# Optimization experiments

Measured on AMD Instinct MI355X. Metric: run time of the kernel, lower is better.

## Reference

```python
import jax, jax.numpy as jnp
import numpy as np

N = 25000      # nodes
E = 250000     # edges (per graph)
D_IN = 256     # input feature dim
H = 4          # heads (both stages)
D = 64         # per-head out dim (hidden_size1 == hidden_size2)
NEG_SLOPE = 0.2  # DGL GATConv default leaky_relu slope


def gat_layer(x, W, al, ar, b, src, dst):
    # x: [N, F_in]; W: [F_in, H*D]; al, ar: [H, D]; b: [H*D]
    feat = (x @ W).reshape(N, H, D)                       # [N,H,D]
    el = jnp.einsum('nhd,hd->nh', feat, al)               # [N,H]
    er = jnp.einsum('nhd,hd->nh', feat, ar)               # [N,H]
    e = jax.nn.leaky_relu(el[src] + er[dst], NEG_SLOPE)   # [E,H]
    # edge softmax over incoming edges of each dst node
    m = jax.ops.segment_max(e, dst, num_segments=N)       # [N,H]
    a = jnp.exp(e - m[dst])                               # [E,H]
    s = jax.ops.segment_sum(a, dst, num_segments=N)       # [N,H]
    alpha = a / s[dst]                                    # [E,H]
    out = jax.ops.segment_sum(alpha[:, :, None] * feat[src], dst, num_segments=N)  # [N,H,D]
    return jax.nn.relu(out + b.reshape(1, H, D))


def dot_score(h, u, v):
    # u_dot_v over last dim: h [N,H,D] -> score [E,H,1]
    return jnp.sum(h[u] * h[v], axis=-1, keepdims=True)


def setup_inputs() -> dict:
    key = jax.random.key(0)
    ks = jax.random.split(key, 16)
    x = jax.random.normal(ks[0], (N, D_IN), dtype=jnp.float32)
    src = jax.random.randint(ks[1], (E,), 0, N, dtype=jnp.int32)
    dst = jax.random.randint(ks[2], (E,), 0, N, dtype=jnp.int32)
    neg_src = jax.random.randint(ks[3], (E,), 0, N, dtype=jnp.int32)
    neg_dst = jax.random.randint(ks[4], (E,), 0, N, dtype=jnp.int32)
    sc = 0.1
    params = {}
    fin = D_IN
    for i in range(3):
        k = 5 + 3 * i
        params[f'W{i+1}'] = sc * jax.random.normal(ks[k], (fin, H * D), dtype=jnp.float32)
        params[f'al{i+1}'] = sc * jax.random.normal(ks[k + 1], (H, D), dtype=jnp.float32)
        params[f'ar{i+1}'] = sc * jax.random.normal(ks[k + 2], (H, D), dtype=jnp.float32)
        params[f'b{i+1}'] = jnp.zeros((H * D,), dtype=jnp.float32)
        fin = H * D
    return dict(x=x, src=src, dst=dst, neg_src=neg_src, neg_dst=neg_dst, **params)


def reference(x, src, dst, neg_src, neg_dst,
              W1, al1, ar1, b1, W2, al2, ar2, b2, W3, al3, ar3, b3):
    h = gat_layer(x, W1, al1, ar1, b1, src, dst)
    h = gat_layer(h.reshape(N, -1), W2, al2, ar2, b2, src, dst)
    h = gat_layer(h.reshape(N, -1), W3, al3, ar3, b3, src, dst)  # [N,H,D]
    return dot_score(h, src, dst), dot_score(h, neg_src, neg_dst)
```

## Files before the change

### kernel.cpp

```cpp
#include <hip/hip_runtime.h>
#include <hip/hip_bf16.h>
#include <math.h>

#define N_NODES 25000
#define N_EDGES 250000
#define NH 4
#define F 256
#define NEG_SLOPE 0.2f

typedef float  f32x4 __attribute__((ext_vector_type(4)));
typedef short  s16x8 __attribute__((ext_vector_type(8)));
typedef ushort u16x8 __attribute__((ext_vector_type(8)));

__device__ inline ushort f2bf(float f) {
    uint u = __float_as_uint(f);
    u += 0x7FFF + ((u >> 16) & 1);
    return (ushort)(u >> 16);
}
__device__ inline float bf2f(ushort s) { return __uint_as_float(((uint)s) << 16); }

__global__ __launch_bounds__(256) void k_cast(const float* __restrict__ x,
                                              ushort* __restrict__ xb) {
    int i = blockIdx.x * blockDim.x + threadIdx.x;
    if (i * 4 >= N_NODES * F) return;
    float4 v = *(const float4*)&x[i * 4];
    ushort4 o;
    o.x = f2bf(v.x); o.y = f2bf(v.y); o.z = f2bf(v.z); o.w = f2bf(v.w);
    *(ushort4*)&xb[i * 4] = o;
}

__global__ void k_degree(const int* __restrict__ dst, int* deg) {
    int e = blockIdx.x * blockDim.x + threadIdx.x;
    if (e < N_EDGES) atomicAdd(&deg[dst[e]], 1);
}

__global__ __launch_bounds__(1024) void k_scan(const int* __restrict__ deg, int* rowptr) {
    __shared__ int sums[1024];
    const int CH = 25;
    int t = threadIdx.x;
    int base = t * CH;
    int s = 0;
    for (int i = 0; i < CH; ++i) {
        int idx = base + i;
        if (idx < N_NODES) s += deg[idx];
    }
    sums[t] = s;
    __syncthreads();
    for (int off = 1; off < 1024; off <<= 1) {
        int v = (t >= off) ? sums[t - off] : 0;
        __syncthreads();
        sums[t] += v;
        __syncthreads();
    }
    int prefix = (t == 0) ? 0 : sums[t - 1];
    for (int i = 0; i < CH; ++i) {
        int idx = base + i;
        if (idx < N_NODES) {
            rowptr[idx] = prefix;
            prefix += deg[idx];
        }
    }
    if (t == 1023) rowptr[N_NODES] = prefix;
}

__global__ void k_bucket(const int* __restrict__ src, const int* __restrict__ dst,
                         const int* __restrict__ rowptr, int* cursor, int* esrc) {
    int e = blockIdx.x * blockDim.x + threadIdx.x;
    if (e >= N_EDGES) return;
    int d = dst[e];
    int p = atomicAdd(&cursor[d], 1);
    esrc[rowptr[d] + p] = src[e];
}

__global__ __launch_bounds__(256) void k_wprep(const float* __restrict__ W,
        short* __restrict__ Hi, short* __restrict__ Lo) {
    __shared__ float T[64][65];
    int bk = (blockIdx.x & 3) * 64;
    int bn = (blockIdx.x >> 2) * 64;
    int t = threadIdx.x;
    int r = t >> 6, c = t & 63;
    #pragma unroll
    for (int i = 0; i < 64; i += 4)
        T[r + i][c] = W[(bk + r + i) * 256 + bn + c];
    __syncthreads();
    #pragma unroll
    for (int i = 0; i < 64; i += 4) {
        float w = T[c][r + i];
        ushort h = f2bf(w);
        Hi[(bn + r + i) * 256 + bk + c] = (short)h;
        Lo[(bn + r + i) * 256 + bk + c] = (short)f2bf(w - bf2f(h));
    }
}

__global__ __launch_bounds__(256) void k_gemm(const ushort* __restrict__ A,
        const short* __restrict__ WtHi, const short* __restrict__ WtLo,
        const float* __restrict__ alv, const float* __restrict__ arv,
        ushort* __restrict__ Cbf, float* __restrict__ el, float* __restrict__ er,
        int M) {
    __shared__ short As[2][64][32];
    __shared__ short WsH[2][256][32], WsL[2][256][32];
    int tid = threadIdx.x;
    int w = tid >> 6, l = tid & 63;
    int row0 = blockIdx.x * 64;

    f32x4 acc[4][4];
    #pragma unroll
    for (int i = 0; i < 4; ++i)
        #pragma unroll
        for (int j = 0; j < 4; ++j)
            acc[i][j] = (f32x4){0.f, 0.f, 0.f, 0.f};

    const int sr = tid >> 2;
    const int sk = tid & 3;
    const int sa = sk ^ ((sr >> 1) & 3);

    s16x8 aReg;
    s16x8 whr[4], wlr[4];

    {
        int gr = row0 + sr;
        aReg = (s16x8){0,0,0,0,0,0,0,0};
        if (gr < M) aReg = *(const s16x8*)&A[gr * 256 + sk * 8];
        #pragma unroll
        for (int r = 0; r < 4; ++r) {
            int n = sr + 64 * r;
            whr[r] = *(const s16x8*)&WtHi[n * 256 + sk * 8];
            wlr[r] = *(const s16x8*)&WtLo[n * 256 + sk * 8];
        }
        *(s16x8*)&As[0][sr][sa * 8] = aReg;
        #pragma unroll
        for (int r = 0; r < 4; ++r) {
            int n = sr + 64 * r;
            int sw = sk ^ ((n >> 1) & 3);
            *(s16x8*)&WsH[0][n][sw * 8] = whr[r];
            *(s16x8*)&WsL[0][n][sw * 8] = wlr[r];
        }
    }
    __syncthreads();

    const int r16 = l & 15, kg = l >> 4;
    for (int c = 0; c < 8; ++c) {
        const int b = c & 1;
        if (c < 7) {
            int kc = (c + 1) * 32;
            int gr = row0 + sr;
            aReg = (s16x8){0,0,0,0,0,0,0,0};
            if (gr < M) aReg = *(const s16x8*)&A[gr * 256 + kc + sk * 8];
            #pragma unroll
            for (int r = 0; r < 4; ++r) {
                int n = sr + 64 * r;
                whr[r] = *(const s16x8*)&WtHi[n * 256 + kc + sk * 8];
                wlr[r] = *(const s16x8*)&WtLo[n * 256 + kc + sk * 8];
            }
        }
        s16x8 ah[4], bh[4], blo[4];
        #pragma unroll
        for (int i = 0; i < 4; ++i) {
            int r = i * 16 + r16;
            int s = (kg ^ ((r >> 1) & 3)) * 8;
            ah[i] = *(const s16x8*)&As[b][r][s];
        }
        #pragma unroll
        for (int j = 0; j < 4; ++j) {
            int cc = w * 64 + j * 16 + r16;
            int s = (kg ^ ((cc >> 1) & 3)) * 8;
            bh[j]  = *(const s16x8*)&WsH[b][cc][s];
            blo[j] = *(const s16x8*)&WsL[b][cc][s];
        }
        #pragma unroll
        for (int i = 0; i < 4; ++i)
            #pragma unroll
            for (int j = 0; j < 4; ++j) {
                acc[i][j] = __builtin_amdgcn_mfma_f32_16x16x32_bf16(ah[i], bh[j],  acc[i][j], 0, 0, 0);
                acc[i][j] = __builtin_amdgcn_mfma_f32_16x16x32_bf16(ah[i], blo[j], acc[i][j], 0, 0, 0);
            }
        if (c < 7) {
            *(s16x8*)&As[b ^ 1][sr][sa * 8] = aReg;
            #pragma unroll
            for (int r = 0; r < 4; ++r) {
                int n = sr + 64 * r;
                int sw = sk ^ ((n >> 1) & 3);
                *(s16x8*)&WsH[b ^ 1][n][sw * 8] = whr[r];
                *(s16x8*)&WsL[b ^ 1][n][sw * 8] = wlr[r];
            }
        }
        __syncthreads();
    }

    float ac4[4], rc4[4];
    #pragma unroll
    for (int j = 0; j < 4; ++j) {
        ac4[j] = alv[w * 64 + j * 16 + r16];
        rc4[j] = arv[w * 64 + j * 16 + r16];
    }
    #pragma unroll
    for (int i = 0; i < 4; ++i) {
        #pragma unroll
        for (int q = 0; q < 4; ++q) {
            int gr = row0 + i * 16 + kg * 4 + q;
            float pel = 0.f, per = 0.f;
            #pragma unroll
            for (int j = 0; j < 4; ++j) {
                float v = acc[i][j][q];
                pel += v * ac4[j];
                per += v * rc4[j];
            }
            pel += __shfl_xor(pel, 1);  per += __shfl_xor(per, 1);
            pel += __shfl_xor(pel, 2);  per += __shfl_xor(per, 2);
            pel += __shfl_xor(pel, 4);  per += __shfl_xor(per, 4);
            pel += __shfl_xor(pel, 8);  per += __shfl_xor(per, 8);
            if (r16 == 0 && gr < M) {
                el[gr * NH + w] = pel;
                er[gr * NH + w] = per;
            }
        }
    }
    #pragma unroll
    for (int i = 0; i < 4; ++i)
        #pragma unroll
        for (int j = 0; j < 4; ++j) {
            int cc = w * 64 + j * 16 + r16;
            #pragma unroll
            for (int q = 0; q < 4; ++q) {
                int gr = row0 + i * 16 + kg * 4 + q;
                if (gr < M) Cbf[gr * 256 + cc] = f2bf(acc[i][j][q]);
            }
        }
}

__global__ __launch_bounds__(256) void k_node(const ushort* __restrict__ featbf,
        const float* __restrict__ el, const float* __restrict__ er,
        const int* __restrict__ rowptr, const int* __restrict__ esrc,
        const float* __restrict__ bias,
        ushort* __restrict__ hbf) {
    int t = threadIdx.x;
    int n = blockIdx.x * 2 + (t >> 7);
    if (n >= N_NODES) return;
    int tt = t & 127;
    int c0 = tt * 2;
    int h = tt >> 5;
    float ern = er[n * NH + h];
    int r0 = rowptr[n], r1 = rowptr[n + 1];
    float acc0 = 0.f, acc1 = 0.f, S = 0.f;
    int i = r0;
    for (; i + 2 <= r1; i += 2) {
        int s0 = esrc[i], s1 = esrc[i + 1];
        uint p0 = *(const uint*)&featbf[s0 * F + c0];
        uint p1 = *(const uint*)&featbf[s1 * F + c0];
        float e0 = el[s0 * NH + h] + ern;
        float e1 = el[s1 * NH + h] + ern;
        e0 = e0 > 0.f ? e0 : NEG_SLOPE * e0;
        e1 = e1 > 0.f ? e1 : NEG_SLOPE * e1;
        float a0 = __expf(e0), a1 = __expf(e1);
        S += a0 + a1;
        acc0 += a0 * bf2f((ushort)(p0 & 0xFFFF)) + a1 * bf2f((ushort)(p1 & 0xFFFF));
        acc1 += a0 * bf2f((ushort)(p0 >> 16))    + a1 * bf2f((ushort)(p1 >> 16));
    }
    if (i < r1) {
        int s0 = esrc[i];
        uint p0 = *(const uint*)&featbf[s0 * F + c0];
        float e0 = el[s0 * NH + h] + ern;
        e0 = e0 > 0.f ? e0 : NEG_SLOPE * e0;
        float a0 = __expf(e0);
        S += a0;
        acc0 += a0 * bf2f((ushort)(p0 & 0xFFFF));
        acc1 += a0 * bf2f((ushort)(p0 >> 16));
    }
    float inv = S > 0.f ? 1.f / S : 0.f;
    float o0 = acc0 * inv + bias[c0];
    float o1 = acc1 * inv + bias[c0 + 1];
    o0 = o0 > 0.f ? o0 : 0.f;
    o1 = o1 > 0.f ? o1 : 0.f;
    uint pk = (uint)f2bf(o0) | ((uint)f2bf(o1) << 16);
    *(uint*)&hbf[n * F + c0] = pk;
}

__global__ __launch_bounds__(256) void k_score(const ushort* __restrict__ h,
        const int* __restrict__ src, const int* __restrict__ dst,
        const int* __restrict__ nsrc, const int* __restrict__ ndst,
        float* __restrict__ out) {
    int g = blockIdx.x * 16 + (threadIdx.x >> 4);
    int sub = threadIdx.x & 15;
    int u, v;
    float* o;
    if (g < N_EDGES) {
        u = src[g]; v = dst[g]; o = out + (size_t)g * NH;
    } else {
        int e = g - N_EDGES;
        u = nsrc[e]; v = ndst[e];
        o = out + (size_t)(N_EDGES + e) * NH;
    }
    u16x8 a0 = *(const u16x8*)&h[u * F + sub * 16];
    u16x8 a1 = *(const u16x8*)&h[u * F + sub * 16 + 8];
    u16x8 b0 = *(const u16x8*)&h[v * F + sub * 16];
    u16x8 b1 = *(const u16x8*)&h[v * F + sub * 16 + 8];
    float p = 0.f;
    #pragma unroll
    for (int i = 0; i < 8; ++i) {
        p += bf2f(a0[i]) * bf2f(b0[i]);
        p += bf2f(a1[i]) * bf2f(b1[i]);
    }
    p += __shfl_xor(p, 1);
    p += __shfl_xor(p, 2);
    if ((sub & 3) == 0) o[sub >> 2] = p;
}

extern "C" void kernel_launch(void* const* d_in, const int* in_sizes, int n_in,
                              void* d_out, int out_size, void* d_ws, size_t ws_size,
                              hipStream_t stream) {
    const float* x    = (const float*)d_in[0];
    const int* src    = (const int*)d_in[1];
    const int* dst    = (const int*)d_in[2];
    const int* nsrc   = (const int*)d_in[3];
    const int* ndst   = (const int*)d_in[4];
    const float* W[3]  = {(const float*)d_in[5], (const float*)d_in[9],  (const float*)d_in[13]};
    const float* al[3] = {(const float*)d_in[6], (const float*)d_in[10], (const float*)d_in[14]};
    const float* ar[3] = {(const float*)d_in[7], (const float*)d_in[11], (const float*)d_in[15]};
    const float* bs[3] = {(const float*)d_in[8], (const float*)d_in[12], (const float*)d_in[16]};

    char* p = (char*)d_ws;
    auto alloc = [&](size_t bytes) {
        char* r = p;
        p += (bytes + 255) & ~size_t(255);
        return r;
    };
    ushort* xbf    = (ushort*)alloc(sizeof(ushort) * N_NODES * F);
    ushort* featbf = (ushort*)alloc(sizeof(ushort) * N_NODES * F);
    ushort* hA     = (ushort*)alloc(sizeof(ushort) * N_NODES * F);
    ushort* hB     = (ushort*)alloc(sizeof(ushort) * N_NODES * F);
    float* el    = (float*)alloc(sizeof(float) * N_NODES * NH);
    float* er    = (float*)alloc(sizeof(float) * N_NODES * NH);
    int* deg     = (int*)alloc(sizeof(int) * N_NODES);
    int* cursor  = (int*)alloc(sizeof(int) * N_NODES);
    int* rowptr  = (int*)alloc(sizeof(int) * (N_NODES + 1));
    int* esrc    = (int*)alloc(sizeof(int) * N_EDGES);
    short* wtHi[3], *wtLo[3];
    for (int i = 0; i < 3; ++i) {
        wtHi[i] = (short*)alloc(sizeof(short) * 256 * 256);
        wtLo[i] = (short*)alloc(sizeof(short) * 256 * 256);
    }

    (void)hipMemsetAsync(deg, 0, sizeof(int) * N_NODES, stream);
    (void)hipMemsetAsync(cursor, 0, sizeof(int) * N_NODES, stream);

    int eb = (N_EDGES + 255) / 256;
    k_cast<<<(N_NODES * F / 4 + 255) / 256, 256, 0, stream>>>(x, xbf);
    k_degree<<<eb, 256, 0, stream>>>(dst, deg);
    k_scan<<<1, 1024, 0, stream>>>(deg, rowptr);
    k_bucket<<<eb, 256, 0, stream>>>(src, dst, rowptr, cursor, esrc);
    for (int L = 0; L < 3; ++L)
        k_wprep<<<16, 256, 0, stream>>>(W[L], wtHi[L], wtLo[L]);

    const ushort* in_h = xbf;
    ushort* outs[3] = {hA, hB, hA};
    int gemm_grid = (N_NODES + 63) / 64;
    int node_grid = (N_NODES + 1) / 2;
    for (int L = 0; L < 3; ++L) {
        k_gemm<<<gemm_grid, 256, 0, stream>>>(in_h, wtHi[L], wtLo[L], al[L], ar[L],
                                              featbf, el, er, N_NODES);
        k_node<<<node_grid, 256, 0, stream>>>(featbf, el, er, rowptr, esrc, bs[L], outs[L]);
        in_h = outs[L];
    }
    k_score<<<(2 * N_EDGES) / 16, 256, 0, stream>>>(outs[2], src, dst, nsrc, ndst, (float*)d_out);
}
```

Before: 400.9 us.

## Drop split-bf16 weight correction, unroll node aggregation by four, score edges in dst order

The GEMM no longer keeps a hi/lo bf16 split of the weights. It uses a single bf16 weight copy, which halves the MFMA count and the weight shared-memory traffic but gives up the extra weight precision. The node aggregation loop now handles four edges per iteration so more gathers are in flight. Positive-edge scoring walks edges in CSR order, using new edst/eid arrays that k_bucket writes, so the h[v] reads are local. Outputs are scattered back through eid.

```diff
diff --git a/kernel.cpp b/kernel.cpp
--- a/kernel.cpp
+++ b/kernel.cpp
@@ -64,16 +64,20 @@
 }
 
 __global__ void k_bucket(const int* __restrict__ src, const int* __restrict__ dst,
-                         const int* __restrict__ rowptr, int* cursor, int* esrc) {
+                         const int* __restrict__ rowptr, int* cursor,
+                         int* esrc, int* edst, int* eid) {
     int e = blockIdx.x * blockDim.x + threadIdx.x;
     if (e >= N_EDGES) return;
     int d = dst[e];
     int p = atomicAdd(&cursor[d], 1);
-    esrc[rowptr[d] + p] = src[e];
+    int slot = rowptr[d] + p;
+    esrc[slot] = src[e];
+    edst[slot] = d;
+    eid[slot]  = e;
 }
 
 __global__ __launch_bounds__(256) void k_wprep(const float* __restrict__ W,
-        short* __restrict__ Hi, short* __restrict__ Lo) {
+        short* __restrict__ Hi) {
     __shared__ float T[64][65];
     int bk = (blockIdx.x & 3) * 64;
     int bn = (blockIdx.x >> 2) * 64;
@@ -86,19 +90,17 @@
     #pragma unroll
     for (int i = 0; i < 64; i += 4) {
         float w = T[c][r + i];
-        ushort h = f2bf(w);
-        Hi[(bn + r + i) * 256 + bk + c] = (short)h;
-        Lo[(bn + r + i) * 256 + bk + c] = (short)f2bf(w - bf2f(h));
+        Hi[(bn + r + i) * 256 + bk + c] = (short)f2bf(w);
     }
 }
 
 __global__ __launch_bounds__(256) void k_gemm(const ushort* __restrict__ A,
-        const short* __restrict__ WtHi, const short* __restrict__ WtLo,
+        const short* __restrict__ Wt,
         const float* __restrict__ alv, const float* __restrict__ arv,
         ushort* __restrict__ Cbf, float* __restrict__ el, float* __restrict__ er,
         int M) {
     __shared__ short As[2][64][32];
-    __shared__ short WsH[2][256][32], WsL[2][256][32];
+    __shared__ short Ws[2][256][32];
     int tid = threadIdx.x;
     int w = tid >> 6, l = tid & 63;
     int row0 = blockIdx.x * 64;
@@ -115,7 +117,7 @@
     const int sa = sk ^ ((sr >> 1) & 3);
 
     s16x8 aReg;
-    s16x8 whr[4], wlr[4];
+    s16x8 whr[4];
 
     {
         int gr = row0 + sr;
@@ -124,16 +126,14 @@
         #pragma unroll
         for (int r = 0; r < 4; ++r) {
             int n = sr + 64 * r;
-            whr[r] = *(const s16x8*)&WtHi[n * 256 + sk * 8];
-            wlr[r] = *(const s16x8*)&WtLo[n * 256 + sk * 8];
+            whr[r] = *(const s16x8*)&Wt[n * 256 + sk * 8];
         }
         *(s16x8*)&As[0][sr][sa * 8] = aReg;
         #pragma unroll
         for (int r = 0; r < 4; ++r) {
             int n = sr + 64 * r;
             int sw = sk ^ ((n >> 1) & 3);
-            *(s16x8*)&WsH[0][n][sw * 8] = whr[r];
-            *(s16x8*)&WsL[0][n][sw * 8] = wlr[r];
+            *(s16x8*)&Ws[0][n][sw * 8] = whr[r];
         }
     }
     __syncthreads();
@@ -149,11 +149,10 @@
             #pragma unroll
             for (int r = 0; r < 4; ++r) {
                 int n = sr + 64 * r;
-                whr[r] = *(const s16x8*)&WtHi[n * 256 + kc + sk * 8];
-                wlr[r] = *(const s16x8*)&WtLo[n * 256 + kc + sk * 8];
-            }
-        }
-        s16x8 ah[4], bh[4], blo[4];
+                whr[r] = *(const s16x8*)&Wt[n * 256 + kc + sk * 8];
+            }
+        }
+        s16x8 ah[4], bh[4];
         #pragma unroll
         for (int i = 0; i < 4; ++i) {
             int r = i * 16 + r16;
@@ -164,24 +163,20 @@
         for (int j = 0; j < 4; ++j) {
             int cc = w * 64 + j * 16 + r16;
             int s = (kg ^ ((cc >> 1) & 3)) * 8;
-            bh[j]  = *(const s16x8*)&WsH[b][cc][s];
-            blo[j] = *(const s16x8*)&WsL[b][cc][s];
+            bh[j] = *(const s16x8*)&Ws[b][cc][s];
         }
         #pragma unroll
         for (int i = 0; i < 4; ++i)
             #pragma unroll
-            for (int j = 0; j < 4; ++j) {
-                acc[i][j] = __builtin_amdgcn_mfma_f32_16x16x32_bf16(ah[i], bh[j],  acc[i][j], 0, 0, 0);
-                acc[i][j] = __builtin_amdgcn_mfma_f32_16x16x32_bf16(ah[i], blo[j], acc[i][j], 0, 0, 0);
-            }
+            for (int j = 0; j < 4; ++j)
+                acc[i][j] = __builtin_amdgcn_mfma_f32_16x16x32_bf16(ah[i], bh[j], acc[i][j], 0, 0, 0);
         if (c < 7) {
             *(s16x8*)&As[b ^ 1][sr][sa * 8] = aReg;
             #pragma unroll
             for (int r = 0; r < 4; ++r) {
                 int n = sr + 64 * r;
                 int sw = sk ^ ((n >> 1) & 3);
-                *(s16x8*)&WsH[b ^ 1][n][sw * 8] = whr[r];
-                *(s16x8*)&WsL[b ^ 1][n][sw * 8] = wlr[r];
+                *(s16x8*)&Ws[b ^ 1][n][sw * 8] = whr[r];
             }
         }
         __syncthreads();
@@ -243,20 +238,28 @@
     int r0 = rowptr[n], r1 = rowptr[n + 1];
     float acc0 = 0.f, acc1 = 0.f, S = 0.f;
     int i = r0;
-    for (; i + 2 <= r1; i += 2) {
-        int s0 = esrc[i], s1 = esrc[i + 1];
+    for (; i + 4 <= r1; i += 4) {
+        int s0 = esrc[i], s1 = esrc[i + 1], s2 = esrc[i + 2], s3 = esrc[i + 3];
         uint p0 = *(const uint*)&featbf[s0 * F + c0];
         uint p1 = *(const uint*)&featbf[s1 * F + c0];
+        uint p2 = *(const uint*)&featbf[s2 * F + c0];
+        uint p3 = *(const uint*)&featbf[s3 * F + c0];
         float e0 = el[s0 * NH + h] + ern;
         float e1 = el[s1 * NH + h] + ern;
+        float e2 = el[s2 * NH + h] + ern;
+        float e3 = el[s3 * NH + h] + ern;
         e0 = e0 > 0.f ? e0 : NEG_SLOPE * e0;
         e1 = e1 > 0.f ? e1 : NEG_SLOPE * e1;
-        float a0 = __expf(e0), a1 = __expf(e1);
-        S += a0 + a1;
-        acc0 += a0 * bf2f((ushort)(p0 & 0xFFFF)) + a1 * bf2f((ushort)(p1 & 0xFFFF));
-        acc1 += a0 * bf2f((ushort)(p0 >> 16))    + a1 * bf2f((ushort)(p1 >> 16));
-    }
-    if (i < r1) {
+        e2 = e2 > 0.f ? e2 : NEG_SLOPE * e2;
+        e3 = e3 > 0.f ? e3 : NEG_SLOPE * e3;
+        float a0 = __expf(e0), a1 = __expf(e1), a2 = __expf(e2), a3 = __expf(e3);
+        S += (a0 + a1) + (a2 + a3);
+        acc0 += a0 * bf2f((ushort)(p0 & 0xFFFF)) + a1 * bf2f((ushort)(p1 & 0xFFFF))
+              + a2 * bf2f((ushort)(p2 & 0xFFFF)) + a3 * bf2f((ushort)(p3 & 0xFFFF));
+        acc1 += a0 * bf2f((ushort)(p0 >> 16))    + a1 * bf2f((ushort)(p1 >> 16))
+              + a2 * bf2f((ushort)(p2 >> 16))    + a3 * bf2f((ushort)(p3 >> 16));
+    }
+    for (; i < r1; ++i) {
         int s0 = esrc[i];
         uint p0 = *(const uint*)&featbf[s0 * F + c0];
         float e0 = el[s0 * NH + h] + ern;
@@ -276,7 +279,8 @@
 }
 
 __global__ __launch_bounds__(256) void k_score(const ushort* __restrict__ h,
-        const int* __restrict__ src, const int* __restrict__ dst,
+        const int* __restrict__ esrc, const int* __restrict__ edst,
+        const int* __restrict__ eid,
         const int* __restrict__ nsrc, const int* __restrict__ ndst,
         float* __restrict__ out) {
     int g = blockIdx.x * 16 + (threadIdx.x >> 4);
@@ -284,7 +288,8 @@
     int u, v;
     float* o;
     if (g < N_EDGES) {
-        u = src[g]; v = dst[g]; o = out + (size_t)g * NH;
+        u = esrc[g]; v = edst[g];
+        o = out + (size_t)eid[g] * NH;
     } else {
         int e = g - N_EDGES;
         u = nsrc[e]; v = ndst[e];
@@ -334,11 +339,11 @@
     int* cursor  = (int*)alloc(sizeof(int) * N_NODES);
     int* rowptr  = (int*)alloc(sizeof(int) * (N_NODES + 1));
     int* esrc    = (int*)alloc(sizeof(int) * N_EDGES);
-    short* wtHi[3], *wtLo[3];
-    for (int i = 0; i < 3; ++i) {
-        wtHi[i] = (short*)alloc(sizeof(short) * 256 * 256);
-        wtLo[i] = (short*)alloc(sizeof(short) * 256 * 256);
-    }
+    int* edst    = (int*)alloc(sizeof(int) * N_EDGES);
+    int* eid     = (int*)alloc(sizeof(int) * N_EDGES);
+    short* wt[3];
+    for (int i = 0; i < 3; ++i)
+        wt[i] = (short*)alloc(sizeof(short) * 256 * 256);
 
     (void)hipMemsetAsync(deg, 0, sizeof(int) * N_NODES, stream);
     (void)hipMemsetAsync(cursor, 0, sizeof(int) * N_NODES, stream);
@@ -347,19 +352,19 @@
     k_cast<<<(N_NODES * F / 4 + 255) / 256, 256, 0, stream>>>(x, xbf);
     k_degree<<<eb, 256, 0, stream>>>(dst, deg);
     k_scan<<<1, 1024, 0, stream>>>(deg, rowptr);
-    k_bucket<<<eb, 256, 0, stream>>>(src, dst, rowptr, cursor, esrc);
+    k_bucket<<<eb, 256, 0, stream>>>(src, dst, rowptr, cursor, esrc, edst, eid);
     for (int L = 0; L < 3; ++L)
-        k_wprep<<<16, 256, 0, stream>>>(W[L], wtHi[L], wtLo[L]);
+        k_wprep<<<16, 256, 0, stream>>>(W[L], wt[L]);
 
     const ushort* in_h = xbf;
     ushort* outs[3] = {hA, hB, hA};
     int gemm_grid = (N_NODES + 63) / 64;
     int node_grid = (N_NODES + 1) / 2;
     for (int L = 0; L < 3; ++L) {
-        k_gemm<<<gemm_grid, 256, 0, stream>>>(in_h, wtHi[L], wtLo[L], al[L], ar[L],
+        k_gemm<<<gemm_grid, 256, 0, stream>>>(in_h, wt[L], al[L], ar[L],
                                               featbf, el, er, N_NODES);
         k_node<<<node_grid, 256, 0, stream>>>(featbf, el, er, rowptr, esrc, bs[L], outs[L]);
         in_h = outs[L];
     }
-    k_score<<<(2 * N_EDGES) / 16, 256, 0, stream>>>(outs[2], src, dst, nsrc, ndst, (float*)d_out);
-}
+    k_score<<<(2 * N_EDGES) / 16, 256, 0, stream>>>(outs[2], esrc, edst, eid, nsrc, ndst, (float*)d_out);
+}
```

New measurement: 367.9 us. 1.09x faster.
